# Kernel optimization log

Measured on AMD Instinct MI355X. Metric: run time of the kernel, lower is better.

## Reference

```python
import jax, jax.numpy as jnp
import numpy as np

EPS = 1e-4  # matches normalize()/pixel_norm eps in the torch source
MP_T = 0.3  # mp_add mixing coefficient


def _weight_norm_1x1(w):
    # w: [out, in, 1, 1]; normalize each output filter (dims 1..3), alpha = 1/sqrt(fan_in),
    # then divide by sqrt(fan_in) as in Conv2d.forward (eval mode: no in-place copy).
    fan_in = w.shape[1] * w.shape[2] * w.shape[3]
    inv_sqrt_fan = np.float32(1.0 / np.sqrt(fan_in))
    n = jnp.sqrt(jnp.sum(w * w, axis=(1, 2, 3), keepdims=True))
    w_hat = w / (EPS + inv_sqrt_fan * n)
    return w_hat * inv_sqrt_fan


def _conv1x1(x, w):
    # 1x1 conv == channel GEMM
    return jnp.einsum('oc,bchw->bohw', _weight_norm_1x1(w)[:, :, 0, 0], x)


def _pixel_norm_last(x):
    # x / sqrt(mean(x^2, axis=-1) + eps)
    ms = jnp.mean(x * x, axis=-1, keepdims=True)
    return x * jax.lax.rsqrt(ms + EPS)


def setup_inputs() -> dict:
    key = jax.random.key(0)
    k1, k2, k3 = jax.random.split(key, 3)
    x = jax.random.normal(k1, (2, 256, 64, 64), dtype=jnp.float32)
    w_qkv = jax.random.normal(k2, (768, 256, 1, 1), dtype=jnp.float32)
    w_out = jax.random.normal(k3, (256, 256, 1, 1), dtype=jnp.float32)
    return {"x": x, "w_qkv": w_qkv, "w_out": w_out, "num_heads": 8}


def reference(x, w_qkv, w_out, num_heads):
    b, c, h, w = x.shape
    head_dim = c // num_heads
    qkv = _conv1x1(x, w_qkv)                      # [b, 3c, h, w]
    q, k, v = jnp.split(qkv, 3, axis=1)           # each [b, c, h, w]

    def to_heads(t):
        # [b, c, h, w] -> [b, heads, hw, head_dim]
        return t.reshape(b, num_heads, head_dim, h * w).transpose(0, 1, 3, 2)

    q = _pixel_norm_last(to_heads(q))
    k = _pixel_norm_last(to_heads(k))
    v = _pixel_norm_last(to_heads(v))

    scale = np.float32(1.0 / np.sqrt(head_dim))
    scores = jnp.einsum('bhqd,bhkd->bhqk', q, k) * scale
    attn = jax.nn.softmax(scores, axis=-1)
    y = jnp.einsum('bhqk,bhkd->bhqd', attn, v)    # [b, heads, hw, head_dim]
    y = y.transpose(0, 1, 3, 2).reshape(b, c, h, w)
    y = _conv1x1(y, w_out)

    # mp_add(x, y, t=0.3)
    t = np.float32(MP_T)
    inv_scale = np.float32(1.0 / np.sqrt(MP_T ** 2 + (1.0 - MP_T) ** 2))
    return ((1.0 - t) * x + t * y) * inv_scale
```

## Files before the change

kernel.cpp:

```cpp
#include <hip/hip_runtime.h>
#include <hip/hip_bf16.h>
#include <math.h>

#define S 4096
#define CIN 256
#define C3 768
#define NH 8
#define HD 32
#define KSPLIT 4

static constexpr float EPS = 1e-4f;

typedef __attribute__((ext_vector_type(8))) __bf16 bf16x8;
typedef __attribute__((ext_vector_type(4))) float f32x4;
typedef __attribute__((ext_vector_type(16))) float f32x16;
typedef __attribute__((ext_vector_type(4))) unsigned u32x4;

static inline __device__ ushort f2bf(float f) {
  unsigned u = __float_as_uint(f);
  return (ushort)((u + 0x7fffu + ((u >> 16) & 1u)) >> 16);
}
static inline __device__ float bf2f(ushort u) {
  return __uint_as_float((unsigned)u << 16);
}

static inline __device__ unsigned cvt_pk_bf16(float lo, float hi) {
  unsigned r;
  asm("v_cvt_pk_bf16_f32 %0, %1, %2" : "=v"(r) : "v"(lo), "v"(hi));
  return r;
}
static inline __device__ void plane32_swap(unsigned& a, unsigned& b) {
  asm("v_permlane32_swap_b32 %0, %1" : "+v"(a), "+v"(b));
}

#define EXP2 __builtin_amdgcn_exp2f


static inline __device__ void s_to_pf(const f32x16 s, bf16x8& plo, bf16x8& phi,
                                      float& lacc) {
  float e0 = EXP2(s[0]), e1 = EXP2(s[1]), e2 = EXP2(s[2]), e3 = EXP2(s[3]);
  float e4 = EXP2(s[4]), e5 = EXP2(s[5]), e6 = EXP2(s[6]), e7 = EXP2(s[7]);
  float e8 = EXP2(s[8]), e9 = EXP2(s[9]), e10 = EXP2(s[10]), e11 = EXP2(s[11]);
  float e12 = EXP2(s[12]), e13 = EXP2(s[13]), e14 = EXP2(s[14]), e15 = EXP2(s[15]);
  lacc += (((e0 + e1) + (e2 + e3)) + ((e4 + e5) + (e6 + e7))) +
          (((e8 + e9) + (e10 + e11)) + ((e12 + e13) + (e14 + e15)));
  unsigned c0 = cvt_pk_bf16(e0, e1);
  unsigned c1 = cvt_pk_bf16(e2, e3);
  unsigned c2 = cvt_pk_bf16(e4, e5);
  unsigned c3 = cvt_pk_bf16(e6, e7);
  plane32_swap(c0, c2);
  plane32_swap(c1, c3);
  u32x4 lo4 = {c0, c1, c2, c3};
  plo = __builtin_bit_cast(bf16x8, lo4);
  unsigned c4 = cvt_pk_bf16(e8, e9);
  unsigned c5 = cvt_pk_bf16(e10, e11);
  unsigned c6 = cvt_pk_bf16(e12, e13);
  unsigned c7 = cvt_pk_bf16(e14, e15);
  plane32_swap(c4, c6);
  plane32_swap(c5, c7);
  u32x4 hi4 = {c4, c5, c6, c7};
  phi = __builtin_bit_cast(bf16x8, hi4);
}

__global__ __launch_bounds__(256) void wnorm_kernel(const float* __restrict__ w_qkv,
                                                    const float* __restrict__ w_out,
                                                    ushort* __restrict__ wqb,
                                                    ushort* __restrict__ wob) {
  const int row = blockIdx.x * 4 + (threadIdx.x >> 6);
  const int lane = threadIdx.x & 63;
  const bool is_q = row < C3;
  const int r2 = is_q ? row : row - C3;
  const float* wr = (is_q ? w_qkv : w_out) + (size_t)r2 * CIN;
  float v[4];
  #pragma unroll
  for (int i = 0; i < 4; i++) v[i] = wr[lane + 64 * i];
  float ss = v[0] * v[0] + v[1] * v[1] + v[2] * v[2] + v[3] * v[3];
  #pragma unroll
  for (int off = 32; off > 0; off >>= 1) ss += __shfl_down(ss, off, 64);
  ss = __shfl(ss, 0, 64);
  const float scale = 1.0f / (sqrtf(ss) + 16.0f * EPS);
  ushort* whr = (is_q ? wqb : wob);
  #pragma unroll
  for (int i = 0; i < 4; i++) {
    const int c = lane + 64 * i;
    whr[((size_t)(r2 >> 4) * (CIN / 32) + (c >> 5)) * 512 + (r2 & 15) * 32 + (c & 31)] =
        f2bf(v[i] * scale);
  }
}

__global__ __launch_bounds__(256) void xt_kernel(const float* __restrict__ X,
                                                 ushort* __restrict__ Xt) {
  const int b = blockIdx.z;
  const int s0 = blockIdx.x * 64, c0 = blockIdx.y * 64;
  __shared__ ushort T[64][72];
  const int tc = threadIdx.x >> 4;
  const int ts = threadIdx.x & 15;
  #pragma unroll
  for (int i = 0; i < 4; i++) {
    const float4 v = *(const float4*)&X[((size_t)(b * CIN + c0 + tc + 16 * i)) * S + s0 + ts * 4];
    ushort4 u;
    u.x = f2bf(v.x); u.y = f2bf(v.y); u.z = f2bf(v.z); u.w = f2bf(v.w);
    *(ushort4*)&T[tc + 16 * i][ts * 4] = u;
  }
  __syncthreads();
  #pragma unroll
  for (int i = 0; i < 4; i++) {
    const int sr = tc + 16 * i;
    const int s = s0 + sr;
    const int c = c0 + ts * 4;
    ushort4 u;
    u.x = T[ts * 4 + 0][sr];
    u.y = T[ts * 4 + 1][sr];
    u.z = T[ts * 4 + 2][sr];
    u.w = T[ts * 4 + 3][sr];
    *(ushort4*)&Xt[(((size_t)b * (S / 16) + (s >> 4)) * (CIN / 32) + (c >> 5)) * 512 +
                   (s & 15) * 32 + (c & 31)] = u;
  }
}

__global__ __launch_bounds__(256) void conv1_fused_kernel(const ushort* __restrict__ W,
                                                          const ushort* __restrict__ Bm,
                                                          ushort* __restrict__ Qn,
                                                          ushort* __restrict__ Kn,
                                                          ushort* __restrict__ Vt) {
  const int b = blockIdx.z;
  const int wid = threadIdx.x >> 6, lane = threadIdx.x & 63;
  const int col = lane & 15, quad = lane >> 4;
  const int m0 = blockIdx.y * 64 + (wid >> 1) * 32;
  const int n0 = blockIdx.x * 128 + (wid & 1) * 64;
  const ushort* Bb = Bm + (size_t)b * (S / 16) * (CIN / 32) * 512;
  const int lofs = col * 32 + quad * 8;
  f32x4 acc[2][4] = {};
  #pragma unroll
  for (int k0 = 0; k0 < CIN; k0 += 32) {
    bf16x8 af[2], bf[4];
    #pragma unroll
    for (int mi = 0; mi < 2; mi++)
      af[mi] = *(const bf16x8*)&W[((size_t)(m0 / 16 + mi) * (CIN / 32) + (k0 >> 5)) * 512 + lofs];
    #pragma unroll
    for (int ni = 0; ni < 4; ni++)
      bf[ni] = *(const bf16x8*)&Bb[((size_t)(n0 / 16 + ni) * (CIN / 32) + (k0 >> 5)) * 512 + lofs];
    #pragma unroll
    for (int mi = 0; mi < 2; mi++)
      #pragma unroll
      for (int ni = 0; ni < 4; ni++)
        acc[mi][ni] = __builtin_amdgcn_mfma_f32_16x16x32_bf16(af[mi], bf[ni], acc[mi][ni], 0, 0, 0);
  }

  const int g = m0 >> 5;
  const int h = g & 7;
  float rn[4];
  #pragma unroll
  for (int ni = 0; ni < 4; ni++) {
    float ss = 0.f;
    #pragma unroll
    for (int mi = 0; mi < 2; mi++)
      #pragma unroll
      for (int r = 0; r < 4; r++) ss += acc[mi][ni][r] * acc[mi][ni][r];
    ss += __shfl_xor(ss, 16, 64);
    ss += __shfl_xor(ss, 32, 64);
    rn[ni] = rsqrtf(ss * (1.0f / HD) + EPS);
    if (g < 8) rn[ni] *= 0.2550348190698169f;
  }

  if (g < 8) {
    ushort* dst = Qn + (size_t)(b * NH + h) * S * HD;
    #pragma unroll
    for (int mi = 0; mi < 2; mi++)
      #pragma unroll
      for (int ni = 0; ni < 4; ni++) {
        ushort4 u;
        u.x = f2bf(acc[mi][ni][0] * rn[ni]);
        u.y = f2bf(acc[mi][ni][1] * rn[ni]);
        u.z = f2bf(acc[mi][ni][2] * rn[ni]);
        u.w = f2bf(acc[mi][ni][3] * rn[ni]);
        *(ushort4*)&dst[(size_t)(n0 + ni * 16 + col) * HD + mi * 16 + quad * 4] = u;
      }
  } else if (g < 16) {
    ushort* dst = Kn + (size_t)(b * NH + h) * S * HD + (size_t)(n0 >> 5) * 1024;
    #pragma unroll
    for (int mi = 0; mi < 2; mi++)
      #pragma unroll
      for (int ni = 0; ni < 4; ni++) {
        ushort4 u;
        u.x = f2bf(acc[mi][ni][0] * rn[ni]);
        u.y = f2bf(acc[mi][ni][1] * rn[ni]);
        u.z = f2bf(acc[mi][ni][2] * rn[ni]);
        u.w = f2bf(acc[mi][ni][3] * rn[ni]);
        *(ushort4*)&dst[(ni >> 1) * 1024 + mi * 512 + ((ni & 1) * 16 + col) * 16 +
                        (quad >> 1) * 8 + (quad & 1) * 4] = u;
      }
  } else {
    ushort* dst = Vt + (size_t)(b * NH + h) * HD * S + (size_t)(n0 >> 6) * 2048;
    #pragma unroll
    for (int mi = 0; mi < 2; mi++)
      #pragma unroll
      for (int ni = 0; ni < 4; ni++)
        #pragma unroll
        for (int r = 0; r < 4; r++)
          dst[ni * 512 + (mi * 16 + quad * 4 + r) * 16 + col] =
              f2bf(acc[mi][ni][r] * rn[ni]);
  }
}

__global__ __launch_bounds__(256, 4) void attn_kernel(const ushort* __restrict__ Qn,
                                                      const ushort* __restrict__ Kn,
                                                      const ushort* __restrict__ Vt,
                                                      ushort* __restrict__ accPb,
                                                      float* __restrict__ lP) {
  const int NWG = (S / 256) * NH * KSPLIT * 2;
  const int bid = blockIdx.x;
  const int id = (bid & 7) * (NWG / 8) + (bid >> 3);
  const int qt = id & 15;
  const int grp = id >> 4;
  const int h = grp & 7;
  const int kp = (grp >> 3) & (KSPLIT - 1);
  const int b = (grp >> 3) / KSPLIT;
  const int wid = threadIdx.x >> 6, lane = threadIdx.x & 63;
  const int ln = lane & 31, hi = lane >> 5;
  const int qA = qt * 256 + wid * 64;
  const int qB = qA + 32;

  const ushort* Qh = Qn + (size_t)(b * NH + h) * S * HD;

  bf16x8 qfA0 = *(const bf16x8*)&Qh[(size_t)(qA + ln) * HD + hi * 8];
  bf16x8 qfA1 = *(const bf16x8*)&Qh[(size_t)(qA + ln) * HD + 16 + hi * 8];
  bf16x8 qfB0 = *(const bf16x8*)&Qh[(size_t)(qB + ln) * HD + hi * 8];
  bf16x8 qfB1 = *(const bf16x8*)&Qh[(size_t)(qB + ln) * HD + 16 + hi * 8];

  const f32x16 z = {};
  f32x16 accA = {}, accB = {};
  float laccA = 0.f, laccB = 0.f;

  const int kt0 = kp * (S / KSPLIT);
  const int loff = (ln * 2 + hi) * 8;
  const ushort* Kp = Kn + (size_t)(b * NH + h) * S * HD + (size_t)kt0 * 32 + loff;
  const ushort* Vp = Vt + (size_t)(b * NH + h) * HD * S + (size_t)kt0 * 32 + loff;

  bf16x8 kf0 = *(const bf16x8*)&Kp[0];
  bf16x8 kf1 = *(const bf16x8*)&Kp[512];
  bf16x8 vf0 = *(const bf16x8*)&Vp[0];
  bf16x8 vf1 = *(const bf16x8*)&Vp[512];

  #pragma unroll 2
  for (int it = 0; it < S / KSPLIT / 32; ++it) {
    f32x16 sA = __builtin_amdgcn_mfma_f32_32x32x16_bf16(kf0, qfA0, z, 0, 0, 0);
    sA = __builtin_amdgcn_mfma_f32_32x32x16_bf16(kf1, qfA1, sA, 0, 0, 0);
    f32x16 sB = __builtin_amdgcn_mfma_f32_32x32x16_bf16(kf0, qfB0, z, 0, 0, 0);
    sB = __builtin_amdgcn_mfma_f32_32x32x16_bf16(kf1, qfB1, sB, 0, 0, 0);
    Kp += 1024;
    kf0 = *(const bf16x8*)&Kp[0];
    kf1 = *(const bf16x8*)&Kp[512];

    bf16x8 pfA0, pfA1;
    s_to_pf(sA, pfA0, pfA1, laccA);
    accA = __builtin_amdgcn_mfma_f32_32x32x16_bf16(vf0, pfA0, accA, 0, 0, 0);
    accA = __builtin_amdgcn_mfma_f32_32x32x16_bf16(vf1, pfA1, accA, 0, 0, 0);

    bf16x8 pfB0, pfB1;
    s_to_pf(sB, pfB0, pfB1, laccB);
    accB = __builtin_amdgcn_mfma_f32_32x32x16_bf16(vf0, pfB0, accB, 0, 0, 0);
    accB = __builtin_amdgcn_mfma_f32_32x32x16_bf16(vf1, pfB1, accB, 0, 0, 0);

    Vp += 1024;
    vf0 = *(const bf16x8*)&Vp[0];
    vf1 = *(const bf16x8*)&Vp[512];
  }

  ushort* ap = accPb + ((size_t)((kp * 2 + b) * NH + h)) * S * HD;
  const size_t rowA = (size_t)(qA + ln) * HD;
  const size_t rowB = (size_t)(qB + ln) * HD;
  #pragma unroll
  for (int g = 0; g < 4; g++) {
    uint2 u;
    u.x = cvt_pk_bf16(accA[4 * g + 0], accA[4 * g + 1]);
    u.y = cvt_pk_bf16(accA[4 * g + 2], accA[4 * g + 3]);
    *(uint2*)&ap[rowA + g * 8 + hi * 4] = u;
    uint2 v;
    v.x = cvt_pk_bf16(accB[4 * g + 0], accB[4 * g + 1]);
    v.y = cvt_pk_bf16(accB[4 * g + 2], accB[4 * g + 3]);
    *(uint2*)&ap[rowB + g * 8 + hi * 4] = v;
  }
  const float lsA = laccA + __shfl_xor(laccA, 32, 64);
  const float lsB = laccB + __shfl_xor(laccB, 32, 64);
  if (hi == 0) {
    float* lp = lP + ((size_t)((kp * 2 + b) * NH + h)) * S;
    lp[qA + ln] = lsA;
    lp[qB + ln] = lsB;
  }
}

__global__ __launch_bounds__(256) void combine_kernel(const ushort* __restrict__ accPb,
                                                      const float* __restrict__ lP,
                                                      ushort* __restrict__ Yt) {
  const int tid = blockIdx.x * 256 + threadIdx.x;
  const int dg = tid & 7;
  const int q = (tid >> 3) & (S - 1);
  const int h = (tid >> 15) & 7;
  const int b = tid >> 18;
  const size_t i0 = ((size_t)(b * NH + h)) * S + q;
  const size_t part = (size_t)2 * NH * S;
  float sx = 0.f, sy = 0.f, sz = 0.f, sw = 0.f, L = 0.f;
  #pragma unroll
  for (int p = 0; p < KSPLIT; p++) {
    const ushort4 a = *(const ushort4*)&accPb[(size_t)p * part * HD + i0 * HD + dg * 4];
    sx += bf2f(a.x); sy += bf2f(a.y); sz += bf2f(a.z); sw += bf2f(a.w);
    L += lP[(size_t)p * part + i0];
  }
  const float rl = 1.0f / L;
  ushort4 o;
  o.x = f2bf(sx * rl);
  o.y = f2bf(sy * rl);
  o.z = f2bf(sz * rl);
  o.w = f2bf(sw * rl);
  *(ushort4*)&Yt[(((size_t)b * (S / 16) + (q >> 4)) * (CIN / 32) + h) * 512 +
                 (q & 15) * 32 + dg * 4] = o;
}

__global__ __launch_bounds__(256) void conv2_kernel(const ushort* __restrict__ W,
                                                    const ushort* __restrict__ Bm,
                                                    const float* __restrict__ RES,
                                                    float* __restrict__ OUT) {
  const int b = blockIdx.z;
  const int wid = threadIdx.x >> 6, lane = threadIdx.x & 63;
  const int col = lane & 15, quad = lane >> 4;
  const int m0 = blockIdx.y * 64 + (wid >> 1) * 32;
  const int n0 = blockIdx.x * 64 + (wid & 1) * 32;
  const ushort* Bb = Bm + (size_t)b * (S / 16) * (CIN / 32) * 512;
  const int lofs = col * 32 + quad * 8;
  f32x4 acc[2][2] = {};
  #pragma unroll
  for (int k0 = 0; k0 < CIN; k0 += 32) {
    bf16x8 af[2], bf[2];
    #pragma unroll
    for (int mi = 0; mi < 2; mi++)
      af[mi] = *(const bf16x8*)&W[((size_t)(m0 / 16 + mi) * (CIN / 32) + (k0 >> 5)) * 512 + lofs];
    #pragma unroll
    for (int ni = 0; ni < 2; ni++)
      bf[ni] = *(const bf16x8*)&Bb[((size_t)(n0 / 16 + ni) * (CIN / 32) + (k0 >> 5)) * 512 + lofs];
    #pragma unroll
    for (int mi = 0; mi < 2; mi++)
      #pragma unroll
      for (int ni = 0; ni < 2; ni++)
        acc[mi][ni] = __builtin_amdgcn_mfma_f32_16x16x32_bf16(af[mi], bf[ni], acc[mi][ni], 0, 0, 0);
  }
  const float tc = 0.3f, om = 0.7f, inv = 1.3130643285972254f;
  #pragma unroll
  for (int mi = 0; mi < 2; mi++)
    #pragma unroll
    for (int ni = 0; ni < 2; ni++)
      #pragma unroll
      for (int r = 0; r < 4; r++) {
        const size_t idx = ((size_t)(b * CIN + m0 + mi * 16 + quad * 4 + r)) * S + n0 + ni * 16 + col;
        OUT[idx] = (om * RES[idx] + tc * acc[mi][ni][r]) * inv;
      }
}

extern "C" void kernel_launch(void* const* d_in, const int* in_sizes, int n_in,
                              void* d_out, int out_size, void* d_ws, size_t ws_size,
                              hipStream_t stream) {
  const float* x = (const float*)d_in[0];
  const float* w_qkv = (const float*)d_in[1];
  const float* w_out = (const float*)d_in[2];
  float* out = (float*)d_out;

  ushort* p = (ushort*)d_ws;
  ushort* wqb = p; p += (size_t)C3 * CIN;
  ushort* wob = p; p += (size_t)CIN * CIN;
  ushort* Qn = p; p += (size_t)2 * NH * S * HD;
  ushort* Kn = p; p += (size_t)2 * NH * S * HD;
  ushort* Vt = p; p += (size_t)2 * NH * S * HD;
  ushort* Yt = p; p += (size_t)2 * S * CIN;
  ushort* R = p; p += (size_t)KSPLIT * 2 * NH * S * HD;
  ushort* Xt = R;
  ushort* accPb = R;
  float* lP = (float*)p;

  wnorm_kernel<<<(C3 + CIN) / 4, 256, 0, stream>>>(w_qkv, w_out, wqb, wob);
  xt_kernel<<<dim3(S / 64, CIN / 64, 2), 256, 0, stream>>>(x, Xt);
  conv1_fused_kernel<<<dim3(S / 128, C3 / 64, 2), 256, 0, stream>>>(wqb, Xt, Qn, Kn, Vt);
  attn_kernel<<<(S / 256) * NH * KSPLIT * 2, 256, 0, stream>>>(Qn, Kn, Vt, accPb, lP);
  combine_kernel<<<2048, 256, 0, stream>>>(accPb, lP, Yt);
  conv2_kernel<<<dim3(S / 64, CIN / 64, 2), 256, 0, stream>>>(wob, Yt, x, out);
}
```

Measured before the change: 143.3 us.

## Fuse split-K combine into conv2 and merge weight-norm with x transpose

Merges the weight-normalization and input-transpose kernels into one launch partitioned by block index. Folds the split-K attention combine into the output projection GEMM, so conv2 reads partial accumulators and row sums directly, normalizes them and packs them as the B operand. This removes two kernel launches and the Yt intermediate write and read. In exchange, each n tile's combine is recomputed by the four M-dimension blocks, raising partial-buffer reads. Residual loads are hoisted before the GEMM loop.

```diff
diff --git a/kernel.cpp b/kernel.cpp
--- a/kernel.cpp
+++ b/kernel.cpp
@@ -62,59 +62,62 @@
   phi = __builtin_bit_cast(bf16x8, hi4);
 }
 
-__global__ __launch_bounds__(256) void wnorm_kernel(const float* __restrict__ w_qkv,
-                                                    const float* __restrict__ w_out,
-                                                    ushort* __restrict__ wqb,
-                                                    ushort* __restrict__ wob) {
-  const int row = blockIdx.x * 4 + (threadIdx.x >> 6);
-  const int lane = threadIdx.x & 63;
-  const bool is_q = row < C3;
-  const int r2 = is_q ? row : row - C3;
-  const float* wr = (is_q ? w_qkv : w_out) + (size_t)r2 * CIN;
-  float v[4];
-  #pragma unroll
-  for (int i = 0; i < 4; i++) v[i] = wr[lane + 64 * i];
-  float ss = v[0] * v[0] + v[1] * v[1] + v[2] * v[2] + v[3] * v[3];
-  #pragma unroll
-  for (int off = 32; off > 0; off >>= 1) ss += __shfl_down(ss, off, 64);
-  ss = __shfl(ss, 0, 64);
-  const float scale = 1.0f / (sqrtf(ss) + 16.0f * EPS);
-  ushort* whr = (is_q ? wqb : wob);
-  #pragma unroll
-  for (int i = 0; i < 4; i++) {
-    const int c = lane + 64 * i;
-    whr[((size_t)(r2 >> 4) * (CIN / 32) + (c >> 5)) * 512 + (r2 & 15) * 32 + (c & 31)] =
-        f2bf(v[i] * scale);
-  }
-}
-
-__global__ __launch_bounds__(256) void xt_kernel(const float* __restrict__ X,
-                                                 ushort* __restrict__ Xt) {
-  const int b = blockIdx.z;
-  const int s0 = blockIdx.x * 64, c0 = blockIdx.y * 64;
+__global__ __launch_bounds__(256) void wnxt_kernel(const float* __restrict__ w_qkv,
+                                                   const float* __restrict__ w_out,
+                                                   ushort* __restrict__ wqb,
+                                                   ushort* __restrict__ wob,
+                                                   const float* __restrict__ X,
+                                                   ushort* __restrict__ Xt) {
   __shared__ ushort T[64][72];
-  const int tc = threadIdx.x >> 4;
-  const int ts = threadIdx.x & 15;
-  #pragma unroll
-  for (int i = 0; i < 4; i++) {
-    const float4 v = *(const float4*)&X[((size_t)(b * CIN + c0 + tc + 16 * i)) * S + s0 + ts * 4];
-    ushort4 u;
-    u.x = f2bf(v.x); u.y = f2bf(v.y); u.z = f2bf(v.z); u.w = f2bf(v.w);
-    *(ushort4*)&T[tc + 16 * i][ts * 4] = u;
-  }
-  __syncthreads();
-  #pragma unroll
-  for (int i = 0; i < 4; i++) {
-    const int sr = tc + 16 * i;
-    const int s = s0 + sr;
-    const int c = c0 + ts * 4;
-    ushort4 u;
-    u.x = T[ts * 4 + 0][sr];
-    u.y = T[ts * 4 + 1][sr];
-    u.z = T[ts * 4 + 2][sr];
-    u.w = T[ts * 4 + 3][sr];
-    *(ushort4*)&Xt[(((size_t)b * (S / 16) + (s >> 4)) * (CIN / 32) + (c >> 5)) * 512 +
-                   (s & 15) * 32 + (c & 31)] = u;
+  if (blockIdx.x < 256) {
+    const int row = blockIdx.x * 4 + (threadIdx.x >> 6);
+    const int lane = threadIdx.x & 63;
+    const bool is_q = row < C3;
+    const int r2 = is_q ? row : row - C3;
+    const float* wr = (is_q ? w_qkv : w_out) + (size_t)r2 * CIN;
+    float v[4];
+    #pragma unroll
+    for (int i = 0; i < 4; i++) v[i] = wr[lane + 64 * i];
+    float ss = v[0] * v[0] + v[1] * v[1] + v[2] * v[2] + v[3] * v[3];
+    #pragma unroll
+    for (int off = 32; off > 0; off >>= 1) ss += __shfl_down(ss, off, 64);
+    ss = __shfl(ss, 0, 64);
+    const float scale = 1.0f / (sqrtf(ss) + 16.0f * EPS);
+    ushort* whr = (is_q ? wqb : wob);
+    #pragma unroll
+    for (int i = 0; i < 4; i++) {
+      const int c = lane + 64 * i;
+      whr[((size_t)(r2 >> 4) * (CIN / 32) + (c >> 5)) * 512 + (r2 & 15) * 32 + (c & 31)] =
+          f2bf(v[i] * scale);
+    }
+  } else {
+    const int bid = blockIdx.x - 256;
+    const int s0 = (bid & 63) * 64;
+    const int c0 = ((bid >> 6) & 3) * 64;
+    const int b = bid >> 8;
+    const int tc = threadIdx.x >> 4;
+    const int ts = threadIdx.x & 15;
+    #pragma unroll
+    for (int i = 0; i < 4; i++) {
+      const float4 v = *(const float4*)&X[((size_t)(b * CIN + c0 + tc + 16 * i)) * S + s0 + ts * 4];
+      ushort4 u;
+      u.x = f2bf(v.x); u.y = f2bf(v.y); u.z = f2bf(v.z); u.w = f2bf(v.w);
+      *(ushort4*)&T[tc + 16 * i][ts * 4] = u;
+    }
+    __syncthreads();
+    #pragma unroll
+    for (int i = 0; i < 4; i++) {
+      const int sr = tc + 16 * i;
+      const int s = s0 + sr;
+      const int c = c0 + ts * 4;
+      ushort4 u;
+      u.x = T[ts * 4 + 0][sr];
+      u.y = T[ts * 4 + 1][sr];
+      u.z = T[ts * 4 + 2][sr];
+      u.w = T[ts * 4 + 3][sr];
+      *(ushort4*)&Xt[(((size_t)b * (S / 16) + (s >> 4)) * (CIN / 32) + (c >> 5)) * 512 +
+                     (s & 15) * 32 + (c & 31)] = u;
+    }
   }
 }
 
@@ -290,35 +293,9 @@
   }
 }
 
-__global__ __launch_bounds__(256) void combine_kernel(const ushort* __restrict__ accPb,
-                                                      const float* __restrict__ lP,
-                                                      ushort* __restrict__ Yt) {
-  const int tid = blockIdx.x * 256 + threadIdx.x;
-  const int dg = tid & 7;
-  const int q = (tid >> 3) & (S - 1);
-  const int h = (tid >> 15) & 7;
-  const int b = tid >> 18;
-  const size_t i0 = ((size_t)(b * NH + h)) * S + q;
-  const size_t part = (size_t)2 * NH * S;
-  float sx = 0.f, sy = 0.f, sz = 0.f, sw = 0.f, L = 0.f;
-  #pragma unroll
-  for (int p = 0; p < KSPLIT; p++) {
-    const ushort4 a = *(const ushort4*)&accPb[(size_t)p * part * HD + i0 * HD + dg * 4];
-    sx += bf2f(a.x); sy += bf2f(a.y); sz += bf2f(a.z); sw += bf2f(a.w);
-    L += lP[(size_t)p * part + i0];
-  }
-  const float rl = 1.0f / L;
-  ushort4 o;
-  o.x = f2bf(sx * rl);
-  o.y = f2bf(sy * rl);
-  o.z = f2bf(sz * rl);
-  o.w = f2bf(sw * rl);
-  *(ushort4*)&Yt[(((size_t)b * (S / 16) + (q >> 4)) * (CIN / 32) + h) * 512 +
-                 (q & 15) * 32 + dg * 4] = o;
-}
-
 __global__ __launch_bounds__(256) void conv2_kernel(const ushort* __restrict__ W,
-                                                    const ushort* __restrict__ Bm,
+                                                    const ushort* __restrict__ accPb,
+                                                    const float* __restrict__ lP,
                                                     const float* __restrict__ RES,
                                                     float* __restrict__ OUT) {
   const int b = blockIdx.z;
@@ -326,18 +303,55 @@
   const int col = lane & 15, quad = lane >> 4;
   const int m0 = blockIdx.y * 64 + (wid >> 1) * 32;
   const int n0 = blockIdx.x * 64 + (wid & 1) * 32;
-  const ushort* Bb = Bm + (size_t)b * (S / 16) * (CIN / 32) * 512;
   const int lofs = col * 32 + quad * 8;
+  const size_t part = (size_t)2 * NH * S;
+
+  float res[2][2][4];
+  #pragma unroll
+  for (int mi = 0; mi < 2; mi++)
+    #pragma unroll
+    for (int ni = 0; ni < 2; ni++)
+      #pragma unroll
+      for (int r = 0; r < 4; r++)
+        res[mi][ni][r] =
+            RES[((size_t)(b * CIN + m0 + mi * 16 + quad * 4 + r)) * S + n0 + ni * 16 + col];
+
   f32x4 acc[2][2] = {};
   #pragma unroll
   for (int k0 = 0; k0 < CIN; k0 += 32) {
+    const int h = k0 >> 5;
     bf16x8 af[2], bf[2];
     #pragma unroll
     for (int mi = 0; mi < 2; mi++)
-      af[mi] = *(const bf16x8*)&W[((size_t)(m0 / 16 + mi) * (CIN / 32) + (k0 >> 5)) * 512 + lofs];
-    #pragma unroll
-    for (int ni = 0; ni < 2; ni++)
-      bf[ni] = *(const bf16x8*)&Bb[((size_t)(n0 / 16 + ni) * (CIN / 32) + (k0 >> 5)) * 512 + lofs];
+      af[mi] = *(const bf16x8*)&W[((size_t)(m0 / 16 + mi) * (CIN / 32) + h) * 512 + lofs];
+    #pragma unroll
+    for (int ni = 0; ni < 2; ni++) {
+      const int q = n0 + ni * 16 + col;
+      const size_t i0 = ((size_t)(b * NH + h)) * S + q;
+      float L = 0.f;
+      float e0 = 0.f, e1 = 0.f, e2 = 0.f, e3 = 0.f;
+      float e4 = 0.f, e5 = 0.f, e6 = 0.f, e7 = 0.f;
+      #pragma unroll
+      for (int p = 0; p < KSPLIT; p++) {
+        const uint4 a = *(const uint4*)&accPb[(size_t)p * part * HD + i0 * HD + quad * 8];
+        e0 += __uint_as_float(a.x << 16);
+        e1 += __uint_as_float(a.x & 0xffff0000u);
+        e2 += __uint_as_float(a.y << 16);
+        e3 += __uint_as_float(a.y & 0xffff0000u);
+        e4 += __uint_as_float(a.z << 16);
+        e5 += __uint_as_float(a.z & 0xffff0000u);
+        e6 += __uint_as_float(a.w << 16);
+        e7 += __uint_as_float(a.w & 0xffff0000u);
+        L += lP[(size_t)p * part + i0];
+      }
+      const float rl = 1.0f / L;
+      u32x4 pk;
+      pk[0] = cvt_pk_bf16(e0 * rl, e1 * rl);
+      pk[1] = cvt_pk_bf16(e2 * rl, e3 * rl);
+      pk[2] = cvt_pk_bf16(e4 * rl, e5 * rl);
+      pk[3] = cvt_pk_bf16(e6 * rl, e7 * rl);
+      bf[ni] = __builtin_bit_cast(bf16x8, pk);
+    }
     #pragma unroll
     for (int mi = 0; mi < 2; mi++)
       #pragma unroll
@@ -352,7 +366,7 @@
       #pragma unroll
       for (int r = 0; r < 4; r++) {
         const size_t idx = ((size_t)(b * CIN + m0 + mi * 16 + quad * 4 + r)) * S + n0 + ni * 16 + col;
-        OUT[idx] = (om * RES[idx] + tc * acc[mi][ni][r]) * inv;
+        OUT[idx] = (om * res[mi][ni][r] + tc * acc[mi][ni][r]) * inv;
       }
 }
 
@@ -370,16 +384,13 @@
   ushort* Qn = p; p += (size_t)2 * NH * S * HD;
   ushort* Kn = p; p += (size_t)2 * NH * S * HD;
   ushort* Vt = p; p += (size_t)2 * NH * S * HD;
-  ushort* Yt = p; p += (size_t)2 * S * CIN;
   ushort* R = p; p += (size_t)KSPLIT * 2 * NH * S * HD;
   ushort* Xt = R;
   ushort* accPb = R;
   float* lP = (float*)p;
 
-  wnorm_kernel<<<(C3 + CIN) / 4, 256, 0, stream>>>(w_qkv, w_out, wqb, wob);
-  xt_kernel<<<dim3(S / 64, CIN / 64, 2), 256, 0, stream>>>(x, Xt);
+  wnxt_kernel<<<256 + 512, 256, 0, stream>>>(w_qkv, w_out, wqb, wob, x, Xt);
   conv1_fused_kernel<<<dim3(S / 128, C3 / 64, 2), 256, 0, stream>>>(wqb, Xt, Qn, Kn, Vt);
   attn_kernel<<<(S / 256) * NH * KSPLIT * 2, 256, 0, stream>>>(Qn, Kn, Vt, accPb, lP);
-  combine_kernel<<<2048, 256, 0, stream>>>(accPb, lP, Yt);
-  conv2_kernel<<<dim3(S / 64, CIN / 64, 2), 256, 0, stream>>>(wob, Yt, x, out);
-}
+  conv2_kernel<<<dim3(S / 64, CIN / 64, 2), 256, 0, stream>>>(wob, accPb, lP, x, out);
+}
```

Result: faster. 139.7 us, median of 2 (-2.5%).
